# Performance work log

Hardware: AMD Instinct MI355X
Metric: run time of the kernel (lower is better)

Reference implementation:

```python
import jax, jax.numpy as jnp
import numpy as np

KS = (5, 5, 5)      # dilated_kernel_size (Kd, Kh, Kw)
STRIDE = (1, 1, 1)
PADDING = (2, 2, 2)
GROUPS = 1


def construct_kernel(W, P, ks):
    # W: (oc, ic/g, kc), P: (3, oc, ic/g, kc)
    Kd, Kh, Kw = ks
    lim = jnp.floor_divide(jnp.array([Kd, Kh, Kw], dtype=P.dtype), 2.0)
    Pp = P + lim[:, None, None, None]          # shift to grid coords
    Pf = jnp.floor(Pp)
    R = Pp - Pf                                # fractional parts, (3, oc, ic, kc)
    P1, P2, P3 = Pf[0], Pf[1], Pf[2]
    R1, R2, R3 = R[0], R[1], R[2]
    # trilinear weights factorize per axis. In the torch original:
    #   L (depth axis, Kd)  compares against P1/R1
    #   I (width axis, Kw)  compares against P2/R2
    #   J (height axis, Kh) compares against P3/R3
    gL = jnp.arange(Kd, dtype=P.dtype)[:, None, None, None]
    gJ = jnp.arange(Kh, dtype=P.dtype)[:, None, None, None]
    gI = jnp.arange(Kw, dtype=P.dtype)[:, None, None, None]
    aL = (gL == P1) * (1.0 - R1) + (gL == P1 + 1.0) * R1   # (Kd, oc, ic, kc)
    aJ = (gJ == P3) * (1.0 - R3) + (gJ == P3 + 1.0) * R3   # (Kh, oc, ic, kc)
    aI = (gI == P2) * (1.0 - R2) + (gI == P2 + 1.0) * R2   # (Kw, oc, ic, kc)
    # K[o,c,l,j,i] = sum_k W[o,c,k] * aL[l,o,c,k] * aJ[j,o,c,k] * aI[i,o,c,k]
    K = jnp.einsum('ock,lock,jock,iock->oclji', W, aL, aJ, aI)
    return K  # (oc, ic/g, Kd, Kh, Kw)


def setup_inputs() -> dict:
    key = jax.random.key(0)
    k1, k2, k3, k4 = jax.random.split(key, 4)
    x = jax.random.normal(k1, (2, 32, 16, 32, 32), dtype=jnp.float32)
    weight = jax.random.normal(k2, (64, 32, 16), dtype=jnp.float32) * 0.05
    P = jax.random.normal(k3, (3, 64, 32, 16), dtype=jnp.float32) * 0.5
    bias = jax.random.normal(k4, (64,), dtype=jnp.float32) * 0.05
    return {"x": x, "weight": weight, "P": P, "bias": bias}


def reference(x, weight, P, bias):
    K = construct_kernel(weight, P, KS)
    out = jax.lax.conv_general_dilated(
        x, K,
        window_strides=STRIDE,
        padding=[(p, p) for p in PADDING],
        dimension_numbers=('NCDHW', 'OIDHW', 'NCDHW'),
        feature_group_count=GROUPS,
    )
    return out + bias[None, :, None, None, None]
```

## Files before the change

kernel.cpp:

```cpp
#include <hip/hip_runtime.h>

#define OC 64
#define IC 32
#define KC 16

typedef __attribute__((ext_vector_type(8))) short bf16x8;
typedef __attribute__((ext_vector_type(16))) float f32x16;

__device__ inline unsigned short f2bf(float f) {
    unsigned u = __builtin_bit_cast(unsigned, f);
    unsigned r = (u + 0x7fffu + ((u >> 16) & 1u)) >> 16;
    return (unsigned short)r;
}

__global__ __launch_bounds__(256) void prep(const float* __restrict__ x,
                                            const float* __restrict__ W,
                                            const float* __restrict__ P,
                                            short* __restrict__ xp,
                                            short* __restrict__ Kb) {
    __shared__ float sR[2][32][36];
    __shared__ float sWP[2][64];
    const int tid = threadIdx.x;
    const int u   = tid >> 7;
    const int ut  = tid & 127;
    const int b   = blockIdx.x;

    if (b < 720) {
        const int ub = b * 2 + u;
        const int n = ub / 720;
        const int rem = ub - n * 720;
        const int z = rem / 36;
        const int h = rem - z * 36;
        const int zr = z - 2, hr = h - 2;
        short* orow = xp + (size_t)((n * 20 + z) * 36 + h) * 1152;
        const bool edge = ((unsigned)zr >= 16u) || ((unsigned)hr >= 32u);

        if (!edge) {
            const float* xb = x + ((size_t)(n * 32) * 16 + zr) * 1024 + hr * 32;
            #pragma unroll
            for (int k = 0; k < 2; ++k) {
                const int id = ut + k * 128;
                const int c = id >> 3, w4 = id & 7;
                const float4 v = *reinterpret_cast<const float4*>(xb + c * 16384 + w4 * 4);
                float* dst = &sR[u][c][2 + w4 * 4];
                *reinterpret_cast<float2*>(dst)     = make_float2(v.x, v.y);
                *reinterpret_cast<float2*>(dst + 2) = make_float2(v.z, v.w);
            }
            {
                const int c = ut >> 2, wz = ut & 3;
                const int w = (wz < 2) ? wz : 32 + wz;
                sR[u][c][w] = 0.f;
            }
        }
        __syncthreads();
        if (edge) {
            for (int idx = ut; idx < 144; idx += 128)
                *reinterpret_cast<float4*>(orow + idx * 8) =
                    make_float4(0.f, 0.f, 0.f, 0.f);
        } else {
            for (int idx = ut; idx < 144; idx += 128) {
                const int cg = idx / 36;
                const int w  = idx - cg * 36;
                bf16x8 pk;
                #pragma unroll
                for (int e = 0; e < 8; ++e) pk[e] = (short)f2bf(sR[u][cg * 8 + e][w]);
                *reinterpret_cast<bf16x8*>(orow + idx * 8) = pk;
            }
        }
    } else {
        const int pair = (b - 720) * 2 + u;
        if (ut < 64)
            sWP[u][ut] = (ut < 16) ? W[pair * 16 + ut]
                                   : P[((ut >> 4) - 1) * 32768 + pair * 16 + (ut & 15)];
        __syncthreads();
        if (ut < 125) {
            const int cell = ut;
            const int l = cell / 25;
            const int j = (cell / 5) % 5;
            const int i = cell % 5;
            const float fl = (float)l, fj = (float)j, fi = (float)i;
            float acc = 0.f;
            #pragma unroll
            for (int k = 0; k < KC; ++k) {
                const float w  = sWP[u][k];
                const float p1 = sWP[u][16 + k] + 2.0f;
                const float p2 = sWP[u][32 + k] + 2.0f;
                const float p3 = sWP[u][48 + k] + 2.0f;
                const float f1 = floorf(p1), r1 = p1 - f1;
                const float f2 = floorf(p2), r2 = p2 - f2;
                const float f3 = floorf(p3), r3 = p3 - f3;
                const float wl = (fl == f1) ? (1.f - r1) : ((fl == f1 + 1.f) ? r1 : 0.f);
                const float wj = (fj == f3) ? (1.f - r3) : ((fj == f3 + 1.f) ? r3 : 0.f);
                const float wi = (fi == f2) ? (1.f - r2) : ((fi == f2 + 1.f) ? r2 : 0.f);
                acc += w * (wl * wj * wi);
            }
            const int o = pair >> 5, c = pair & 31;
            const int og = o >> 5;
            Kb[(size_t)(og * 125 + cell) * 1024 + (c >> 3) * 256 + (o & 31) * 8 + (c & 7)] =
                (short)f2bf(acc);
        }
    }
}

#define ASLOT 25600
#define BBASE 51200
#define BSLOT 13824

__global__ __launch_bounds__(512, 2) void conv_mfma(const short* __restrict__ Kb,
                                                    const short* __restrict__ xp,
                                                    const float* __restrict__ bias,
                                                    float* __restrict__ out) {
    const int sw = (blockIdx.x & 7) * 32 + (blockIdx.x >> 3);
    const int og = sw & 1;
    const int hb = (sw >> 1) & 3;
    const int d  = (sw >> 3) & 15;
    const int n  = sw >> 7;
    const int h0 = hb * 8;

    __shared__ short sL[2 * ASLOT + 2 * BSLOT];

    const int tid  = threadIdx.x;
    const int wv   = tid >> 6;
    const int lane = tid & 63;
    const int wcol = lane & 31;
    const int hi   = lane >> 5;
    const int hp   = wv >> 2;
    const int g    = (wv >> 1) & 1;
    const int s    = (wv ^ (wv >> 2)) & 1;

    const short* srcA0 = Kb + (size_t)(og * 125) * 1024;
    const short* srcB0 = xp + ((size_t)(n * 20 + d) * 36 + h0) * 1152;

    const int aoff = wcol * 8 + (g * 2 + hi) * 256;
    const int boff = (g * 2 + hi) * 288 + wcol * 8;
    const int rb   = 4 * hp;

    f32x16 ac0, ac1, ac2, ac3;
    #pragma unroll
    for (int e = 0; e < 16; ++e) { ac0[e] = 0.f; ac1[e] = 0.f; ac2[e] = 0.f; ac3[e] = 0.f; }

    bf16x8 Aq[2][3];
    bf16x8 Bq[5][3];

#define STAGEA(L, BUF)                                                        \
    {                                                                         \
        const short* s_ = srcA0 + (size_t)(L) * 25600;                        \
        short* d_ = sL + (BUF) * ASLOT;                                       \
        _Pragma("unroll")                                                     \
        for (int k_ = 0; k_ < 6; ++k_) {                                      \
            const int t_ = k_ * 512 + tid;                                    \
            __builtin_amdgcn_global_load_lds(                                 \
                (const __attribute__((address_space(1))) unsigned int*)(s_ + t_ * 8), \
                (__attribute__((address_space(3))) unsigned int*)(d_ + t_ * 8), \
                16, 0, 0);                                                    \
        }                                                                     \
        if (tid < 128) {                                                      \
            const int t_ = 3072 + tid;                                        \
            __builtin_amdgcn_global_load_lds(                                 \
                (const __attribute__((address_space(1))) unsigned int*)(s_ + t_ * 8), \
                (__attribute__((address_space(3))) unsigned int*)(d_ + t_ * 8), \
                16, 0, 0);                                                    \
        }                                                                     \
    }

#define STAGEB(L, BUF)                                                        \
    {                                                                         \
        const short* s_ = srcB0 + (size_t)(L) * 41472;                        \
        short* d_ = sL + BBASE + (BUF) * BSLOT;                               \
        _Pragma("unroll")                                                     \
        for (int k_ = 0; k_ < 3; ++k_) {                                      \
            const int t_ = k_ * 512 + tid;                                    \
            __builtin_amdgcn_global_load_lds(                                 \
                (const __attribute__((address_space(1))) unsigned int*)(s_ + t_ * 8), \
                (__attribute__((address_space(3))) unsigned int*)(d_ + t_ * 8), \
                16, 0, 0);                                                    \
        }                                                                     \
        if (tid < 192) {                                                      \
            const int t_ = 1536 + tid;                                        \
            __builtin_amdgcn_global_load_lds(                                 \
                (const __attribute__((address_space(1))) unsigned int*)(s_ + t_ * 8), \
                (__attribute__((address_space(3))) unsigned int*)(d_ + t_ * 8), \
                16, 0, 0);                                                    \
        }                                                                     \
    }

#define LOADA(PAR, BUF, J, I0, NI)                                            \
    {                                                                         \
        const short* pa_ = sL + (BUF) * ASLOT + ((J) * 5 + (I0)) * 1024 + aoff; \
        _Pragma("unroll")                                                     \
        for (int ii = 0; ii < (NI); ++ii)                                     \
            Aq[PAR][ii] = *reinterpret_cast<const bf16x8*>(pa_ + ii * 1024);  \
    }

#define LOADB(SLOT, BUF, RW, I0, NI)                                          \
    {                                                                         \
        const short* pb_ = sL + BBASE + (BUF) * BSLOT + (rb + (RW)) * 1152 + boff + (I0) * 8; \
        _Pragma("unroll")                                                     \
        for (int ii = 0; ii < (NI); ++ii)                                     \
            Bq[SLOT][ii] = *reinterpret_cast<const bf16x8*>(pb_ + ii * 8);    \
    }

#define MFMA_STEP(J, NI)                                                      \
    {                                                                         \
        __builtin_amdgcn_s_setprio(1);                                        \
        _Pragma("unroll")                                                     \
        for (int ii = 0; ii < (NI); ++ii) {                                   \
            const bf16x8 a_ = Aq[(J) & 1][ii];                                \
            ac0 = __builtin_amdgcn_mfma_f32_32x32x16_bf16(a_, Bq[(J) % 5][ii], ac0, 0, 0, 0);       \
            ac1 = __builtin_amdgcn_mfma_f32_32x32x16_bf16(a_, Bq[((J) + 1) % 5][ii], ac1, 0, 0, 0); \
            ac2 = __builtin_amdgcn_mfma_f32_32x32x16_bf16(a_, Bq[((J) + 2) % 5][ii], ac2, 0, 0, 0); \
            ac3 = __builtin_amdgcn_mfma_f32_32x32x16_bf16(a_, Bq[((J) + 3) % 5][ii], ac3, 0, 0, 0); \
        }                                                                     \
        __builtin_amdgcn_s_setprio(0);                                        \
    }

#define MAIN(I0, NI)                                                          \
    {                                                                         \
        STAGEA(0, 0); STAGEB(0, 0);                                           \
        __syncthreads();                                                      \
        _Pragma("unroll")                                                     \
        for (int l = 0; l < 5; ++l) {                                         \
            const int buf = l & 1;                                            \
            if (l < 4) STAGEA(l + 1, buf ^ 1);                                \
            LOADA(0, buf, 0, I0, NI);                                         \
            LOADB(0, buf, 0, I0, NI);                                         \
            LOADB(1, buf, 1, I0, NI);                                         \
            LOADB(2, buf, 2, I0, NI);                                         \
            LOADB(3, buf, 3, I0, NI);                                         \
            _Pragma("unroll")                                                 \
            for (int j = 0; j < 5; ++j) {                                     \
                if (j < 4) {                                                  \
                    LOADA((j + 1) & 1, buf, j + 1, I0, NI);                   \
                    LOADB((j + 4) % 5, buf, j + 4, I0, NI);                   \
                }                                                             \
                MFMA_STEP(j, NI);                                             \
                if (j == 0 && l < 4) STAGEB(l + 1, buf ^ 1);                  \
            }                                                                 \
            if (l < 4) __syncthreads();                                       \
        }                                                                     \
    }

    if (s == 0) { MAIN(0, 3) } else { MAIN(3, 2) }

#undef STAGEA
#undef STAGEB
#undef LOADA
#undef LOADB
#undef MFMA_STEP
#undef MAIN

    __syncthreads();
    float* sF = reinterpret_cast<float*>(sL);
    const int cls = g * 2 + s;
#define PWRITE(R, A)                                                          \
    {                                                                         \
        float* p_ = sF + ((((cls * 2 + hp) * 4 + (R)) * 4) * 64 + lane) * 4;  \
        _Pragma("unroll")                                                     \
        for (int eg = 0; eg < 4; ++eg) {                                      \
            float4 v_ = make_float4(A[4 * eg], A[4 * eg + 1],                 \
                                    A[4 * eg + 2], A[4 * eg + 3]);            \
            *reinterpret_cast<float4*>(p_ + eg * 256) = v_;                   \
        }                                                                     \
    }
    PWRITE(0, ac0) PWRITE(1, ac1) PWRITE(2, ac2) PWRITE(3, ac3)
#undef PWRITE
    __syncthreads();

    const int hpR = wv >> 2, rR = wv & 3;
    const int h = h0 + wv;
    #pragma unroll
    for (int eg = 0; eg < 4; ++eg) {
        float4 sv = make_float4(0.f, 0.f, 0.f, 0.f);
        #pragma unroll
        for (int c4 = 0; c4 < 4; ++c4) {
            const float4 t = *reinterpret_cast<const float4*>(
                sF + ((((c4 * 2 + hpR) * 4 + rR) * 4 + eg) * 64 + lane) * 4);
            sv.x += t.x; sv.y += t.y; sv.z += t.z; sv.w += t.w;
        }
        #pragma unroll
        for (int k = 0; k < 4; ++k) {
            const int e = eg * 4 + k;
            const int o = og * 32 + (e & 3) + 8 * (e >> 2) + 4 * hi;
            const float v = (k == 0) ? sv.x : (k == 1) ? sv.y : (k == 2) ? sv.z : sv.w;
            out[((size_t)(n * 64 + o) * 16 + d) * 1024 + h * 32 + wcol] = v + bias[o];
        }
    }
}

extern "C" void kernel_launch(void* const* d_in, const int* in_sizes, int n_in,
                              void* d_out, int out_size, void* d_ws, size_t ws_size,
                              hipStream_t stream) {
    const float* x    = (const float*)d_in[0];
    const float* W    = (const float*)d_in[1];
    const float* P    = (const float*)d_in[2];
    const float* bias = (const float*)d_in[3];
    float* outp = (float*)d_out;

    short* Kb = (short*)d_ws;
    short* xp = (short*)((char*)d_ws + 524288);

    prep<<<1744, 256, 0, stream>>>(x, W, P, xp, Kb);
    conv_mfma<<<256, 512, 0, stream>>>(Kb, xp, bias, outp);
}
```

Measured before the change: 25.59 us.

## Halve conv block to 4 waves and drop LDS double buffering

The conv kernel now uses 256-thread blocks covering 4 output rows instead of 512-thread blocks covering 8, and launches twice as many blocks. LDS shrinks to a single buffer for kernel weights and input rows, so each depth slice is staged, synchronised, consumed, then synchronised again, with no prefetch overlap. The aim is higher occupancy and more blocks per device in exchange for exposed load latency, an extra barrier per slice, and more redundant weight staging per output.

New measurement: 28.99 us. 13.3% more time.

```diff
diff --git a/kernel.cpp b/kernel.cpp
--- a/kernel.cpp
+++ b/kernel.cpp
@@ -103,37 +103,35 @@
 }
 
 #define ASLOT 25600
-#define BBASE 51200
-#define BSLOT 13824
-
-__global__ __launch_bounds__(512, 2) void conv_mfma(const short* __restrict__ Kb,
+#define BBASE 25600
+#define BSLOT 9216
+
+__global__ __launch_bounds__(256, 2) void conv_mfma(const short* __restrict__ Kb,
                                                     const short* __restrict__ xp,
                                                     const float* __restrict__ bias,
                                                     float* __restrict__ out) {
-    const int sw = (blockIdx.x & 7) * 32 + (blockIdx.x >> 3);
+    const int sw = (blockIdx.x & 7) * 64 + (blockIdx.x >> 3);
     const int og = sw & 1;
-    const int hb = (sw >> 1) & 3;
-    const int d  = (sw >> 3) & 15;
-    const int n  = sw >> 7;
-    const int h0 = hb * 8;
-
-    __shared__ short sL[2 * ASLOT + 2 * BSLOT];
+    const int hb = (sw >> 1) & 7;
+    const int d  = (sw >> 4) & 15;
+    const int n  = sw >> 8;
+    const int h0 = hb * 4;
+
+    __shared__ short sL[ASLOT + BSLOT];
 
     const int tid  = threadIdx.x;
     const int wv   = tid >> 6;
     const int lane = tid & 63;
     const int wcol = lane & 31;
     const int hi   = lane >> 5;
-    const int hp   = wv >> 2;
-    const int g    = (wv >> 1) & 1;
-    const int s    = (wv ^ (wv >> 2)) & 1;
+    const int g    = wv & 1;
+    const int s    = (wv ^ (wv >> 1)) & 1;
 
     const short* srcA0 = Kb + (size_t)(og * 125) * 1024;
     const short* srcB0 = xp + ((size_t)(n * 20 + d) * 36 + h0) * 1152;
 
     const int aoff = wcol * 8 + (g * 2 + hi) * 256;
     const int boff = (g * 2 + hi) * 288 + wcol * 8;
-    const int rb   = 4 * hp;
 
     f32x16 ac0, ac1, ac2, ac3;
     #pragma unroll
@@ -142,59 +140,57 @@
     bf16x8 Aq[2][3];
     bf16x8 Bq[5][3];
 
-#define STAGEA(L, BUF)                                                        \
+#define STAGEA(L)                                                             \
     {                                                                         \
         const short* s_ = srcA0 + (size_t)(L) * 25600;                        \
-        short* d_ = sL + (BUF) * ASLOT;                                       \
-        _Pragma("unroll")                                                     \
-        for (int k_ = 0; k_ < 6; ++k_) {                                      \
-            const int t_ = k_ * 512 + tid;                                    \
-            __builtin_amdgcn_global_load_lds(                                 \
-                (const __attribute__((address_space(1))) unsigned int*)(s_ + t_ * 8), \
-                (__attribute__((address_space(3))) unsigned int*)(d_ + t_ * 8), \
+        _Pragma("unroll")                                                     \
+        for (int k_ = 0; k_ < 12; ++k_) {                                     \
+            const int t_ = k_ * 256 + tid;                                    \
+            __builtin_amdgcn_global_load_lds(                                 \
+                (const __attribute__((address_space(1))) unsigned int*)(s_ + t_ * 8), \
+                (__attribute__((address_space(3))) unsigned int*)(sL + t_ * 8), \
                 16, 0, 0);                                                    \
         }                                                                     \
         if (tid < 128) {                                                      \
             const int t_ = 3072 + tid;                                        \
             __builtin_amdgcn_global_load_lds(                                 \
                 (const __attribute__((address_space(1))) unsigned int*)(s_ + t_ * 8), \
-                (__attribute__((address_space(3))) unsigned int*)(d_ + t_ * 8), \
-                16, 0, 0);                                                    \
-        }                                                                     \
-    }
-
-#define STAGEB(L, BUF)                                                        \
+                (__attribute__((address_space(3))) unsigned int*)(sL + t_ * 8), \
+                16, 0, 0);                                                    \
+        }                                                                     \
+    }
+
+#define STAGEB(L)                                                             \
     {                                                                         \
         const short* s_ = srcB0 + (size_t)(L) * 41472;                        \
-        short* d_ = sL + BBASE + (BUF) * BSLOT;                               \
-        _Pragma("unroll")                                                     \
-        for (int k_ = 0; k_ < 3; ++k_) {                                      \
-            const int t_ = k_ * 512 + tid;                                    \
-            __builtin_amdgcn_global_load_lds(                                 \
-                (const __attribute__((address_space(1))) unsigned int*)(s_ + t_ * 8), \
-                (__attribute__((address_space(3))) unsigned int*)(d_ + t_ * 8), \
-                16, 0, 0);                                                    \
-        }                                                                     \
-        if (tid < 192) {                                                      \
-            const int t_ = 1536 + tid;                                        \
-            __builtin_amdgcn_global_load_lds(                                 \
-                (const __attribute__((address_space(1))) unsigned int*)(s_ + t_ * 8), \
-                (__attribute__((address_space(3))) unsigned int*)(d_ + t_ * 8), \
-                16, 0, 0);                                                    \
-        }                                                                     \
-    }
-
-#define LOADA(PAR, BUF, J, I0, NI)                                            \
-    {                                                                         \
-        const short* pa_ = sL + (BUF) * ASLOT + ((J) * 5 + (I0)) * 1024 + aoff; \
+        _Pragma("unroll")                                                     \
+        for (int k_ = 0; k_ < 4; ++k_) {                                      \
+            const int t_ = k_ * 256 + tid;                                    \
+            __builtin_amdgcn_global_load_lds(                                 \
+                (const __attribute__((address_space(1))) unsigned int*)(s_ + t_ * 8), \
+                (__attribute__((address_space(3))) unsigned int*)(sL + BBASE + t_ * 8), \
+                16, 0, 0);                                                    \
+        }                                                                     \
+        if (tid < 128) {                                                      \
+            const int t_ = 1024 + tid;                                        \
+            __builtin_amdgcn_global_load_lds(                                 \
+                (const __attribute__((address_space(1))) unsigned int*)(s_ + t_ * 8), \
+                (__attribute__((address_space(3))) unsigned int*)(sL + BBASE + t_ * 8), \
+                16, 0, 0);                                                    \
+        }                                                                     \
+    }
+
+#define LOADA(PAR, J, I0, NI)                                                 \
+    {                                                                         \
+        const short* pa_ = sL + ((J) * 5 + (I0)) * 1024 + aoff;               \
         _Pragma("unroll")                                                     \
         for (int ii = 0; ii < (NI); ++ii)                                     \
             Aq[PAR][ii] = *reinterpret_cast<const bf16x8*>(pa_ + ii * 1024);  \
     }
 
-#define LOADB(SLOT, BUF, RW, I0, NI)                                          \
-    {                                                                         \
-        const short* pb_ = sL + BBASE + (BUF) * BSLOT + (rb + (RW)) * 1152 + boff + (I0) * 8; \
+#define LOADB(SLOT, RW, I0, NI)                                               \
+    {                                                                         \
+        const short* pb_ = sL + BBASE + (RW) * 1152 + boff + (I0) * 8;        \
         _Pragma("unroll")                                                     \
         for (int ii = 0; ii < (NI); ++ii)                                     \
             Bq[SLOT][ii] = *reinterpret_cast<const bf16x8*>(pb_ + ii * 8);    \
@@ -216,27 +212,22 @@
 
 #define MAIN(I0, NI)                                                          \
     {                                                                         \
-        STAGEA(0, 0); STAGEB(0, 0);                                           \
-        __syncthreads();                                                      \
         _Pragma("unroll")                                                     \
         for (int l = 0; l < 5; ++l) {                                         \
-            const int buf = l & 1;                                            \
-            if (l < 4) STAGEA(l + 1, buf ^ 1);                                \
-            LOADA(0, buf, 0, I0, NI);                                         \
-            LOADB(0, buf, 0, I0, NI);                                         \
-            LOADB(1, buf, 1, I0, NI);                                         \
-            LOADB(2, buf, 2, I0, NI);                                         \
-            LOADB(3, buf, 3, I0, NI);                                         \
+            if (l > 0) __syncthreads();     \
+            STAGEA(l); STAGEB(l);                                             \
+            __syncthreads();                \
+            LOADA(0, 0, I0, NI);                                              \
+            LOADB(0, 0, I0, NI); LOADB(1, 1, I0, NI);                         \
+            LOADB(2, 2, I0, NI); LOADB(3, 3, I0, NI);                         \
             _Pragma("unroll")                                                 \
             for (int j = 0; j < 5; ++j) {                                     \
                 if (j < 4) {                                                  \
-                    LOADA((j + 1) & 1, buf, j + 1, I0, NI);                   \
-                    LOADB((j + 4) % 5, buf, j + 4, I0, NI);                   \
+                    LOADA((j + 1) & 1, j + 1, I0, NI);                        \
+                    LOADB((j + 4) % 5, j + 4, I0, NI);                        \
                 }                                                             \
                 MFMA_STEP(j, NI);                                             \
-                if (j == 0 && l < 4) STAGEB(l + 1, buf ^ 1);                  \
             }                                                                 \
-            if (l < 4) __syncthreads();                                       \
         }                                                                     \
     }
 
@@ -254,7 +245,7 @@
     const int cls = g * 2 + s;
 #define PWRITE(R, A)                                                          \
     {                                                                         \
-        float* p_ = sF + ((((cls * 2 + hp) * 4 + (R)) * 4) * 64 + lane) * 4;  \
+        float* p_ = sF + (((cls * 4 + (R)) * 4) * 64 + lane) * 4;             \
         _Pragma("unroll")                                                     \
         for (int eg = 0; eg < 4; ++eg) {                                      \
             float4 v_ = make_float4(A[4 * eg], A[4 * eg + 1],                 \
@@ -266,7 +257,7 @@
 #undef PWRITE
     __syncthreads();
 
-    const int hpR = wv >> 2, rR = wv & 3;
+    const int rR = wv;
     const int h = h0 + wv;
     #pragma unroll
     for (int eg = 0; eg < 4; ++eg) {
@@ -274,7 +265,7 @@
         #pragma unroll
         for (int c4 = 0; c4 < 4; ++c4) {
             const float4 t = *reinterpret_cast<const float4*>(
-                sF + ((((c4 * 2 + hpR) * 4 + rR) * 4 + eg) * 64 + lane) * 4);
+                sF + (((c4 * 4 + rR) * 4 + eg) * 64 + lane) * 4);
             sv.x += t.x; sv.y += t.y; sv.z += t.z; sv.w += t.w;
         }
         #pragma unroll
@@ -300,5 +291,5 @@
     short* xp = (short*)((char*)d_ws + 524288);
 
     prep<<<1744, 256, 0, stream>>>(x, W, P, xp, Kb);
-    conv_mfma<<<256, 512, 0, stream>>>(Kb, xp, bias, outp);
-}
+    conv_mfma<<<512, 256, 0, stream>>>(Kb, xp, bias, outp);
+}
```
